# Performance work log

Hardware: AMD Instinct MI355X
Metric: run time of the kernel (lower is better)

Reference implementation:

```python
import jax, jax.numpy as jnp
import numpy as np

NUM_NODES = 100000
NUM_EDGES = 1600000
DIM = 64
TAU = 0.5
EPS = 1e-12
SURGERY_EPS = 1e-6


def setup_inputs() -> dict:
    key = jax.random.key(0)
    k1, k2, k3, k4, k5 = jax.random.split(key, 5)
    x = jax.random.normal(k1, (NUM_NODES, DIM), dtype=jnp.float32)
    edge_index = jax.random.randint(k2, (2, NUM_EDGES), 0, NUM_NODES, dtype=jnp.int64)
    edge_weight = jax.random.uniform(k3, (NUM_EDGES,), dtype=jnp.float32)
    # nn.Linear weights (no bias): y = x @ W.T
    W_self = jax.random.normal(k4, (DIM, DIM), dtype=jnp.float32) / np.sqrt(DIM)
    W_neigh = jax.random.normal(k5, (DIM, DIM), dtype=jnp.float32) / np.sqrt(DIM)
    return {"x": x, "edge_index": edge_index, "edge_weight": edge_weight,
            "W_self": W_self, "W_neigh": W_neigh}


def reference(x, edge_index, edge_weight, W_self, W_neigh):
    num_nodes = x.shape[0]
    row, col = edge_index[0], edge_index[1]

    # --- Ollivier-Ricci (LLY limit-free combinatorial lower-bound) curvature per edge ---
    deg = jax.ops.segment_sum(edge_weight, row, num_segments=num_nodes)  # weighted out-degree
    inv_du = 1.0 / jnp.maximum(deg[row], EPS)
    inv_dv = 1.0 / jnp.maximum(deg[col], EPS)
    kappa = 2.0 * inv_du + 2.0 * inv_dv - 2.0  # [E]

    # --- CFL-stable step size for the Ricci flow ---
    delta_t = 0.5 / (jnp.max(jnp.abs(kappa)) + 1e-6)

    # --- Ricci-flow half step: dw/dt = -kappa * w ---
    w_half = jnp.maximum(edge_weight * (1.0 - 0.5 * delta_t * kappa), 0.0)

    # --- metric surgery: drop degenerate edges (implemented as a zero-weight mask,
    #     keeping edge count static so the kernel is jit-compatible) ---
    mask = w_half > SURGERY_EPS
    w_half = jnp.where(mask, w_half, 0.0)

    # --- row normalisation ---
    row_sum = jax.ops.segment_sum(w_half, row, num_segments=num_nodes)
    w_norm = w_half / jnp.maximum(row_sum[row], EPS)

    # --- Laplacian off-diagonals: L_uv = -w_norm  =>  -L_uv = w_norm ---
    minus_L = w_norm

    # --- incident mean curvature per node (over surviving edges) -> curvature gate ---
    cnt = jax.ops.segment_sum(mask.astype(x.dtype), row, num_segments=num_nodes)
    k_sum = jax.ops.segment_sum(jnp.where(mask, kappa, 0.0), row, num_segments=num_nodes)
    mean_kappa = k_sum / jnp.maximum(cnt, 1.0)
    rho = jax.nn.sigmoid(mean_kappa)  # [N]

    # --- gated message passing ---
    h_self = x @ W_self.T    # [N, D]
    h_neigh = x @ W_neigh.T  # [N, D]
    msg = minus_L[:, None] * h_neigh[col]                      # [E, D] gather + scale
    neigh_aggr = jax.ops.segment_sum(msg, row, num_segments=num_nodes)  # scatter-add

    # h0 buffer == first-forward x (detached)
    out = rho[:, None] * h_self + neigh_aggr + TAU * x
    return out, edge_index, w_norm
```

## Files before the change

### kernel.cpp

```cpp
#include <hip/hip_runtime.h>
#include <math.h>

#define NNODES 100000
#define NEDGES 1600000
#define DIM 64
#define TAU 0.5f
#define EPSF 1e-12f
#define SEPS 1e-6f

#define K 256
#define RPB 391
#define TILE 4096
#define EPT 16
#define CAP 7168

typedef unsigned long long ull;
typedef unsigned short u16;
typedef __attribute__((ext_vector_type(8))) short bf16x8;
typedef __attribute__((ext_vector_type(4))) float f32x4;

__device__ __forceinline__ float bf2f(u16 h) {
    return __uint_as_float((unsigned)h << 16);
}
__device__ __forceinline__ u16 f2bf(float f) {
    unsigned u = __float_as_uint(f);
    u += 0x7FFFu + ((u >> 16) & 1);
    return (u16)(u >> 16);
}

__global__ __launch_bounds__(256) void k_bcount(const int* __restrict__ ei,
                                                int* __restrict__ bcnt, int E, int N) {
    __shared__ int cnt[K];
    cnt[threadIdx.x] = 0;
    __syncthreads();
    int stride = gridDim.x * blockDim.x;
    for (int e = blockIdx.x * blockDim.x + threadIdx.x; e < E; e += stride) {
        int r = min(max(ei[e], 0), N - 1);
        atomicAdd(&cnt[r / RPB], 1);
    }
    __syncthreads();
    int v = cnt[threadIdx.x];
    if (v) atomicAdd(&bcnt[threadIdx.x], v);
}

__global__ __launch_bounds__(256) void k_bscan(const int* __restrict__ bcnt,
                                               int* __restrict__ bbase, int* __restrict__ bcur,
                                               int* __restrict__ off, int E, int N) {
    __shared__ int sc[K];
    int t = threadIdx.x;
    int v = bcnt[t];
    sc[t] = v;
    __syncthreads();
    for (int o = 1; o < K; o <<= 1) {
        int a = (t >= o) ? sc[t - o] : 0;
        __syncthreads();
        sc[t] += a;
        __syncthreads();
    }
    int ex = sc[t] - v;
    bbase[t] = ex;
    bcur[t] = ex;
    if (t == K - 1) { bbase[K] = sc[t]; off[N] = E; }
}

__global__ __launch_bounds__(256) void k_bin(const int* __restrict__ ei, const float* __restrict__ w,
                                             int* __restrict__ bcur, ull* __restrict__ arena,
                                             int E, int N) {
    __shared__ ull stg[TILE];
    __shared__ unsigned char bkt[TILE];
    __shared__ int cnt[K], lscan[K], gbase[K], cur[K], sc[K];
    __shared__ int tot;
    int t = threadIdx.x;
    int e0 = blockIdx.x * TILE;
    cnt[t] = 0; cur[t] = 0;
    __syncthreads();
    ull rec[EPT];
    int bb[EPT];
#pragma unroll
    for (int j = 0; j < EPT; j++) {
        int e = e0 + t + j * 256;
        bb[j] = -1;
        if (e < E) {
            int r = min(max(ei[e], 0), N - 1);
            int c = min(max(ei[E + e], 0), N - 1);
            float wv = w[e];
            int b = r / RPB, lr = r - b * RPB;
            rec[j] = ((ull)__float_as_uint(wv) << 32) | (unsigned)(c | (lr << 17));
            bb[j] = b;
            atomicAdd(&cnt[b], 1);
        }
    }
    __syncthreads();
    int v = cnt[t];
    sc[t] = v;
    __syncthreads();
    for (int o = 1; o < K; o <<= 1) {
        int a = (t >= o) ? sc[t - o] : 0;
        __syncthreads();
        sc[t] += a;
        __syncthreads();
    }
    lscan[t] = sc[t] - v;
    if (v > 0) gbase[t] = atomicAdd(&bcur[t], v);
    if (t == K - 1) tot = sc[t];
    __syncthreads();
#pragma unroll
    for (int j = 0; j < EPT; j++) {
        if (bb[j] >= 0) {
            int p = lscan[bb[j]] + atomicAdd(&cur[bb[j]], 1);
            stg[p] = rec[j];
            bkt[p] = (unsigned char)bb[j];
        }
    }
    __syncthreads();
    int T = tot;
    for (int i = t; i < T; i += 256) {
        int b = bkt[i];
        arena[(size_t)gbase[b] + (i - lscan[b])] = stg[i];
    }
}

__global__ __launch_bounds__(256) void k_sort(const int* __restrict__ bbase,
                                              ull* __restrict__ arena,
                                              float* __restrict__ invdeg,
                                              int* __restrict__ off, int N) {
    __shared__ ull stg[CAP];
    __shared__ int hist[RPB];
    __shared__ float degl[RPB];
    __shared__ int cur[RPB];
    __shared__ int sc[512];
    int t = threadIdx.x, b = blockIdx.x;
    int base = bbase[b];
    int cnt = min(bbase[b + 1] - base, CAP);
    for (int i = t; i < RPB; i += 256) { hist[i] = 0; degl[i] = 0.0f; cur[i] = 0; }
    __syncthreads();
    for (int i = t; i < cnt; i += 256) {
        ull rec = arena[base + i];
        stg[i] = rec;
        int lr = (int)((rec >> 17) & 0x1FF);
        atomicAdd(&hist[lr], 1);
        atomicAdd(&degl[lr], __uint_as_float((unsigned)(rec >> 32)));
    }
    __syncthreads();
    int v0 = (t < RPB) ? hist[t] : 0;
    int v1 = (t + 256 < RPB) ? hist[t + 256] : 0;
    sc[t] = v0; sc[t + 256] = v1;
    __syncthreads();
    for (int o = 1; o < 512; o <<= 1) {
        int a = (t >= o) ? sc[t - o] : 0;
        int c2 = (t + 256 >= o) ? sc[t + 256 - o] : 0;
        __syncthreads();
        sc[t] += a; sc[t + 256] += c2;
        __syncthreads();
    }
    int ex0 = sc[t] - v0, ex1 = sc[t + 256] - v1;
    hist[t] = ex0;
    if (t + 256 < RPB) hist[t + 256] = ex1;
    int rn0 = b * RPB + t;
    if (rn0 < N) { off[rn0] = base + ex0; invdeg[rn0] = 1.0f / fmaxf(degl[t], EPSF); }
    int rn1 = rn0 + 256;
    if (t + 256 < RPB && rn1 < N) { off[rn1] = base + ex1; invdeg[rn1] = 1.0f / fmaxf(degl[t + 256], EPSF); }
    __syncthreads();
    int2* out2 = (int2*)arena;
    for (int i = t; i < cnt; i += 256) {
        ull rec = stg[i];
        int lr = (int)((rec >> 17) & 0x1FF);
        int p = hist[lr] + atomicAdd(&cur[lr], 1);
        out2[base + p] = make_int2((int)(rec & 0x1FFFF), (int)(unsigned)(rec >> 32));
    }
}

__global__ __launch_bounds__(256) void k_maxk(const int* __restrict__ off, const int2* __restrict__ csr,
                                              const float* __restrict__ invdeg,
                                              float* __restrict__ maxabs, int N) {
    int n = blockIdx.x * 256 + threadIdx.x;
    float m = 0.0f;
    if (n < N) {
        int s = off[n], e = off[n + 1];
        float a = 2.0f * invdeg[n] - 2.0f;
        for (int i = s; i < e; i++) {
            int2 pr = csr[i];
            m = fmaxf(m, fabsf(a + 2.0f * invdeg[pr.x]));
        }
    }
    for (int o = 32; o > 0; o >>= 1) m = fmaxf(m, __shfl_down(m, o, 64));
    __shared__ float red[4];
    int lane = threadIdx.x & 63, wid = threadIdx.x >> 6;
    if (lane == 0) red[wid] = m;
    __syncthreads();
    if (threadIdx.x == 0) {
        float bm = fmaxf(fmaxf(red[0], red[1]), fmaxf(red[2], red[3]));
        atomicMax((unsigned int*)maxabs, __float_as_uint(bm));
    }
}

__global__ void k_node(const int* __restrict__ off, const float* __restrict__ invdeg,
                       int2* __restrict__ csr, const float* __restrict__ maxabs,
                       float* __restrict__ rho, float* __restrict__ row_sum, int N) {
    int n = blockIdx.x * blockDim.x + threadIdx.x;
    if (n >= N) return;
    int s = off[n], e2 = off[n + 1];
    float dt = 0.5f / (*maxabs + 1e-6f);
    float a = 2.0f * invdeg[n] - 2.0f;
    float rs = 0.0f, ct = 0.0f, ks = 0.0f;
    for (int i = s; i < e2; i++) {
        int2 pr = csr[i];
        float we = __int_as_float(pr.y);
        float kap = a + 2.0f * invdeg[pr.x];
        float wh = fmaxf(we * (1.0f - 0.5f * dt * kap), 0.0f);
        float wst = 0.0f;
        if (wh > SEPS) { rs += wh; ct += 1.0f; ks += kap; wst = wh; }
        csr[i] = make_int2(pr.x, __float_as_int(wst));
    }
    float mk = ks / fmaxf(ct, 1.0f);
    rho[n] = 1.0f / (1.0f + expf(-mk));
    row_sum[n] = rs;
}

#define WL(mp, d, kk) (((mp) * 64 + (d)) * 72 + (kk))
__global__ __launch_bounds__(256) void k_gemm(const float* __restrict__ x,
                                              const float* __restrict__ Wself,
                                              const float* __restrict__ Wneigh,
                                              const float* __restrict__ rho,
                                              u16* __restrict__ hneigh_h,
                                              float* __restrict__ out, int N) {
    __shared__ u16 wlds[4 * 64 * 72];
    int t = threadIdx.x;
    for (int i = t; i < 4096; i += 256) {
        int d = i >> 6, k = i & 63;
        float v = Wself[i];
        u16 h = f2bf(v);
        u16 lo = f2bf(v - bf2f(h));
        wlds[WL(0, d, k)] = h;
        wlds[WL(1, d, k)] = lo;
        v = Wneigh[i];
        h = f2bf(v);
        lo = f2bf(v - bf2f(h));
        wlds[WL(2, d, k)] = h;
        wlds[WL(3, d, k)] = lo;
    }
    __syncthreads();
    int w = t >> 6, l = t & 63;
    int m = l & 15, kg = l >> 4;
    int n0 = blockIdx.x * 64 + w * 16;
    if (n0 >= N) return;
    int nodeA = n0 + m;
    bf16x8 ah[2], al[2];
#pragma unroll
    for (int ks = 0; ks < 2; ks++) {
        float v[8];
        if (nodeA < N) {
            const float4* xp = (const float4*)(x + (size_t)nodeA * 64 + ks * 32 + kg * 8);
            float4 v0 = xp[0], v1 = xp[1];
            v[0] = v0.x; v[1] = v0.y; v[2] = v0.z; v[3] = v0.w;
            v[4] = v1.x; v[5] = v1.y; v[6] = v1.z; v[7] = v1.w;
        } else {
#pragma unroll
            for (int j = 0; j < 8; j++) v[j] = 0.0f;
        }
#pragma unroll
        for (int j = 0; j < 8; j++) {
            u16 h = f2bf(v[j]);
            u16 lo = f2bf(v[j] - bf2f(h));
            ah[ks][j] = (short)h;
            al[ks][j] = (short)lo;
        }
    }
    f32x4 accS[4], accN[4];
#pragma unroll
    for (int dt = 0; dt < 4; dt++) {
        accS[dt] = (f32x4){0.0f, 0.0f, 0.0f, 0.0f};
        accN[dt] = (f32x4){0.0f, 0.0f, 0.0f, 0.0f};
    }
#pragma unroll
    for (int dt = 0; dt < 4; dt++) {
        int d = dt * 16 + m;
#pragma unroll
        for (int ks = 0; ks < 2; ks++) {
            int kof = ks * 32 + kg * 8;
            bf16x8 bsh = *(const bf16x8*)&wlds[WL(0, d, kof)];
            bf16x8 bsl = *(const bf16x8*)&wlds[WL(1, d, kof)];
            bf16x8 bnh = *(const bf16x8*)&wlds[WL(2, d, kof)];
            bf16x8 bnl = *(const bf16x8*)&wlds[WL(3, d, kof)];
            accS[dt] = __builtin_amdgcn_mfma_f32_16x16x32_bf16(ah[ks], bsh, accS[dt], 0, 0, 0);
            accS[dt] = __builtin_amdgcn_mfma_f32_16x16x32_bf16(al[ks], bsh, accS[dt], 0, 0, 0);
            accS[dt] = __builtin_amdgcn_mfma_f32_16x16x32_bf16(ah[ks], bsl, accS[dt], 0, 0, 0);
            accN[dt] = __builtin_amdgcn_mfma_f32_16x16x32_bf16(ah[ks], bnh, accN[dt], 0, 0, 0);
            accN[dt] = __builtin_amdgcn_mfma_f32_16x16x32_bf16(al[ks], bnh, accN[dt], 0, 0, 0);
            accN[dt] = __builtin_amdgcn_mfma_f32_16x16x32_bf16(ah[ks], bnl, accN[dt], 0, 0, 0);
        }
    }
    int rbase = kg * 4;
#pragma unroll
    for (int r = 0; r < 4; r++) {
        int nn = n0 + rbase + r;
        if (nn >= N) continue;
        float rh = rho[nn];
#pragma unroll
        for (int dt = 0; dt < 4; dt++) {
            int d = dt * 16 + m;
            size_t idx = (size_t)nn * 64 + d;
            out[idx] = rh * accS[dt][r] + TAU * x[idx];
            hneigh_h[idx] = f2bf(accN[dt][r]);
        }
    }
}

__global__ __launch_bounds__(256) void k_aggr(const int* __restrict__ off,
                                              const int2* __restrict__ csr,
                                              const float* __restrict__ row_sum,
                                              const u16* __restrict__ hneigh_h,
                                              float* __restrict__ out, int N) {
    int t = threadIdx.x;
    int lane = t & 63;
    int q = lane & 15;
    int g = lane >> 4;
    int n = blockIdx.x * 4 + (t >> 6);
    if (n >= N) return;
    int s = off[n], end = off[n + 1];
    float inv_rs = 1.0f / fmaxf(row_sum[n], EPSF);
    const ushort4* hn4 = (const ushort4*)hneigh_h;
    float a0 = 0.0f, a1 = 0.0f, a2 = 0.0f, a3 = 0.0f;
    int i = s;
    for (; i + 16 <= end; i += 16) {
        int2 p0 = csr[i + g];
        int2 p1 = csr[i + 4 + g];
        int2 p2 = csr[i + 8 + g];
        int2 p3 = csr[i + 12 + g];
        ushort4 h0 = hn4[(unsigned)((p0.x << 4) | q)];
        ushort4 h1 = hn4[(unsigned)((p1.x << 4) | q)];
        ushort4 h2 = hn4[(unsigned)((p2.x << 4) | q)];
        ushort4 h3 = hn4[(unsigned)((p3.x << 4) | q)];
        float w0 = __int_as_float(p0.y), w1 = __int_as_float(p1.y);
        float w2 = __int_as_float(p2.y), w3 = __int_as_float(p3.y);
        a0 = fmaf(w0, bf2f(h0.x), a0); a1 = fmaf(w0, bf2f(h0.y), a1);
        a2 = fmaf(w0, bf2f(h0.z), a2); a3 = fmaf(w0, bf2f(h0.w), a3);
        a0 = fmaf(w1, bf2f(h1.x), a0); a1 = fmaf(w1, bf2f(h1.y), a1);
        a2 = fmaf(w1, bf2f(h1.z), a2); a3 = fmaf(w1, bf2f(h1.w), a3);
        a0 = fmaf(w2, bf2f(h2.x), a0); a1 = fmaf(w2, bf2f(h2.y), a1);
        a2 = fmaf(w2, bf2f(h2.z), a2); a3 = fmaf(w2, bf2f(h2.w), a3);
        a0 = fmaf(w3, bf2f(h3.x), a0); a1 = fmaf(w3, bf2f(h3.y), a1);
        a2 = fmaf(w3, bf2f(h3.z), a2); a3 = fmaf(w3, bf2f(h3.w), a3);
    }
    for (; i + 8 <= end; i += 8) {
        int2 p0 = csr[i + g];
        int2 p1 = csr[i + 4 + g];
        ushort4 h0 = hn4[(unsigned)((p0.x << 4) | q)];
        ushort4 h1 = hn4[(unsigned)((p1.x << 4) | q)];
        float w0 = __int_as_float(p0.y), w1 = __int_as_float(p1.y);
        a0 = fmaf(w0, bf2f(h0.x), a0); a1 = fmaf(w0, bf2f(h0.y), a1);
        a2 = fmaf(w0, bf2f(h0.z), a2); a3 = fmaf(w0, bf2f(h0.w), a3);
        a0 = fmaf(w1, bf2f(h1.x), a0); a1 = fmaf(w1, bf2f(h1.y), a1);
        a2 = fmaf(w1, bf2f(h1.z), a2); a3 = fmaf(w1, bf2f(h1.w), a3);
    }
    for (; i < end; i += 4) {
        int e = i + g;
        bool v = e < end;
        int2 p = make_int2(0, 0);
        if (v) p = csr[e];
        ushort4 h = hn4[(unsigned)((p.x << 4) | q)];
        float wv = v ? __int_as_float(p.y) : 0.0f;
        a0 = fmaf(wv, bf2f(h.x), a0);
        a1 = fmaf(wv, bf2f(h.y), a1);
        a2 = fmaf(wv, bf2f(h.z), a2);
        a3 = fmaf(wv, bf2f(h.w), a3);
    }
    a0 += __shfl_xor(a0, 16, 64);
    a1 += __shfl_xor(a1, 16, 64);
    a2 += __shfl_xor(a2, 16, 64);
    a3 += __shfl_xor(a3, 16, 64);
    a0 += __shfl_xor(a0, 32, 64);
    a1 += __shfl_xor(a1, 32, 64);
    a2 += __shfl_xor(a2, 32, 64);
    a3 += __shfl_xor(a3, 32, 64);
    if (g == 0) {
        float4* o4 = (float4*)(out + (size_t)n * 64);
        float4 o = o4[q];
        o.x += a0 * inv_rs;
        o.y += a1 * inv_rs;
        o.z += a2 * inv_rs;
        o.w += a3 * inv_rs;
        o4[q] = o;
    }
}

__global__ void k_final(const int* __restrict__ ei, const float* __restrict__ w,
                        const float* __restrict__ invdeg, const float* __restrict__ row_sum,
                        const float* __restrict__ maxabs,
                        float* __restrict__ out_ei, float* __restrict__ out_wn, int E, int N) {
    int e = blockIdx.x * blockDim.x + threadIdx.x;
    if (e >= E) return;
    int r0 = ei[e], c0 = ei[E + e];
    int r = min(max(r0, 0), N - 1);
    int c = min(max(c0, 0), N - 1);
    float dt = 0.5f / (*maxabs + 1e-6f);
    float kap = 2.0f * invdeg[r] + 2.0f * invdeg[c] - 2.0f;
    float wh = fmaxf(w[e] * (1.0f - 0.5f * dt * kap), 0.0f);
    if (wh <= SEPS) wh = 0.0f;
    out_wn[e] = wh / fmaxf(row_sum[r], EPSF);
    out_ei[e] = (float)r0;
    out_ei[E + e] = (float)c0;
}

extern "C" void kernel_launch(void* const* d_in, const int* in_sizes, int n_in,
                              void* d_out, int out_size, void* d_ws, size_t ws_size,
                              hipStream_t stream) {
    (void)in_sizes; (void)n_in; (void)out_size; (void)ws_size;
    const int N = NNODES, E = NEDGES;

    const float* x      = (const float*)d_in[0];
    const int*   ei     = (const int*)d_in[1];
    const float* w      = (const float*)d_in[2];
    const float* Wself  = (const float*)d_in[3];
    const float* Wneigh = (const float*)d_in[4];

    float* out    = (float*)d_out;
    float* out_ei = out + (size_t)N * DIM;
    float* out_wn = out_ei + 2 * (size_t)E;

    ull*  arena = (ull*)out_ei;
    int2* csr   = (int2*)out_ei;

    float* invdeg  = (float*)d_ws;
    int*   off     = (int*)d_ws + (size_t)N;
    float* rho     = (float*)d_ws + 2 * (size_t)N + 16;
    float* row_sum = rho + (size_t)N;
    float* maxabs  = row_sum + (size_t)N;
    int*   bcnt    = (int*)(maxabs + 4);
    int*   bbase   = bcnt + 256;
    int*   bcur    = bbase + 257;
    u16*   hneigh_h = (u16*)((float*)d_ws + 4 * (size_t)N + 800);

    hipMemsetAsync((void*)maxabs, 0, 260 * sizeof(float), stream);

    k_bcount<<<256, 256, 0, stream>>>(ei, bcnt, E, N);
    k_bscan<<<1, 256, 0, stream>>>(bcnt, bbase, bcur, off, E, N);
    k_bin<<<(E + TILE - 1) / TILE, 256, 0, stream>>>(ei, w, bcur, arena, E, N);
    k_sort<<<K, 256, 0, stream>>>(bbase, arena, invdeg, off, N);
    k_maxk<<<(N + 255) / 256, 256, 0, stream>>>(off, csr, invdeg, maxabs, N);
    k_node<<<(N + 255) / 256, 256, 0, stream>>>(off, invdeg, csr, maxabs, rho, row_sum, N);
    k_gemm<<<(N + 63) / 64, 256, 0, stream>>>(x, Wself, Wneigh, rho, hneigh_h, out, N);
    k_aggr<<<(N + 3) / 4, 256, 0, stream>>>(off, csr, row_sum, hneigh_h, out, N);
    k_final<<<(E + 255) / 256, 256, 0, stream>>>(ei, w, invdeg, row_sum, maxabs,
                                                 out_ei, out_wn, E, N);
}
```

Baseline: 279.7 us.

## Drop bucket count pass via fixed-capacity buckets and recompute edge weights in aggregation

```diff
diff --git a/kernel.cpp b/kernel.cpp
--- a/kernel.cpp
+++ b/kernel.cpp
@@ -28,39 +28,8 @@
     return (u16)(u >> 16);
 }
 
-__global__ __launch_bounds__(256) void k_bcount(const int* __restrict__ ei,
-                                                int* __restrict__ bcnt, int E, int N) {
-    __shared__ int cnt[K];
-    cnt[threadIdx.x] = 0;
-    __syncthreads();
-    int stride = gridDim.x * blockDim.x;
-    for (int e = blockIdx.x * blockDim.x + threadIdx.x; e < E; e += stride) {
-        int r = min(max(ei[e], 0), N - 1);
-        atomicAdd(&cnt[r / RPB], 1);
-    }
-    __syncthreads();
-    int v = cnt[threadIdx.x];
-    if (v) atomicAdd(&bcnt[threadIdx.x], v);
-}
-
-__global__ __launch_bounds__(256) void k_bscan(const int* __restrict__ bcnt,
-                                               int* __restrict__ bbase, int* __restrict__ bcur,
-                                               int* __restrict__ off, int E, int N) {
-    __shared__ int sc[K];
-    int t = threadIdx.x;
-    int v = bcnt[t];
-    sc[t] = v;
-    __syncthreads();
-    for (int o = 1; o < K; o <<= 1) {
-        int a = (t >= o) ? sc[t - o] : 0;
-        __syncthreads();
-        sc[t] += a;
-        __syncthreads();
-    }
-    int ex = sc[t] - v;
-    bbase[t] = ex;
-    bcur[t] = ex;
-    if (t == K - 1) { bbase[K] = sc[t]; off[N] = E; }
+__global__ __launch_bounds__(256) void k_init(int* __restrict__ bcur) {
+    bcur[threadIdx.x] = threadIdx.x * CAP;
 }
 
 __global__ __launch_bounds__(256) void k_bin(const int* __restrict__ ei, const float* __restrict__ w,
@@ -116,22 +85,24 @@
     int T = tot;
     for (int i = t; i < T; i += 256) {
         int b = bkt[i];
-        arena[(size_t)gbase[b] + (i - lscan[b])] = stg[i];
-    }
-}
-
-__global__ __launch_bounds__(256) void k_sort(const int* __restrict__ bbase,
+        size_t pos = (size_t)gbase[b] + (i - lscan[b]);
+        if (pos < (size_t)(b + 1) * CAP) arena[pos] = stg[i];
+    }
+}
+
+__global__ __launch_bounds__(256) void k_sort(const int* __restrict__ bcur,
                                               ull* __restrict__ arena,
                                               float* __restrict__ invdeg,
-                                              int* __restrict__ off, int N) {
+                                              int* __restrict__ off, int* __restrict__ degi,
+                                              int N) {
     __shared__ ull stg[CAP];
     __shared__ int hist[RPB];
     __shared__ float degl[RPB];
     __shared__ int cur[RPB];
     __shared__ int sc[512];
     int t = threadIdx.x, b = blockIdx.x;
-    int base = bbase[b];
-    int cnt = min(bbase[b + 1] - base, CAP);
+    int base = b * CAP;
+    int cnt = min(bcur[b] - base, CAP);
     for (int i = t; i < RPB; i += 256) { hist[i] = 0; degl[i] = 0.0f; cur[i] = 0; }
     __syncthreads();
     for (int i = t; i < cnt; i += 256) {
@@ -157,9 +128,15 @@
     hist[t] = ex0;
     if (t + 256 < RPB) hist[t + 256] = ex1;
     int rn0 = b * RPB + t;
-    if (rn0 < N) { off[rn0] = base + ex0; invdeg[rn0] = 1.0f / fmaxf(degl[t], EPSF); }
+    if (rn0 < N) {
+        off[rn0] = base + ex0; degi[rn0] = v0;
+        invdeg[rn0] = 1.0f / fmaxf(degl[t], EPSF);
+    }
     int rn1 = rn0 + 256;
-    if (t + 256 < RPB && rn1 < N) { off[rn1] = base + ex1; invdeg[rn1] = 1.0f / fmaxf(degl[t + 256], EPSF); }
+    if (t + 256 < RPB && rn1 < N) {
+        off[rn1] = base + ex1; degi[rn1] = v1;
+        invdeg[rn1] = 1.0f / fmaxf(degl[t + 256], EPSF);
+    }
     __syncthreads();
     int2* out2 = (int2*)arena;
     for (int i = t; i < cnt; i += 256) {
@@ -170,18 +147,15 @@
     }
 }
 
-__global__ __launch_bounds__(256) void k_maxk(const int* __restrict__ off, const int2* __restrict__ csr,
+__global__ __launch_bounds__(256) void k_maxk(const int* __restrict__ ei,
                                               const float* __restrict__ invdeg,
-                                              float* __restrict__ maxabs, int N) {
-    int n = blockIdx.x * 256 + threadIdx.x;
+                                              float* __restrict__ maxabs, int E, int N) {
+    int e = blockIdx.x * 256 + threadIdx.x;
     float m = 0.0f;
-    if (n < N) {
-        int s = off[n], e = off[n + 1];
-        float a = 2.0f * invdeg[n] - 2.0f;
-        for (int i = s; i < e; i++) {
-            int2 pr = csr[i];
-            m = fmaxf(m, fabsf(a + 2.0f * invdeg[pr.x]));
-        }
+    if (e < E) {
+        int r = min(max(ei[e], 0), N - 1);
+        int c = min(max(ei[E + e], 0), N - 1);
+        m = fabsf(2.0f * invdeg[r] + 2.0f * invdeg[c] - 2.0f);
     }
     for (int o = 32; o > 0; o >>= 1) m = fmaxf(m, __shfl_down(m, o, 64));
     __shared__ float red[4];
@@ -194,12 +168,13 @@
     }
 }
 
-__global__ void k_node(const int* __restrict__ off, const float* __restrict__ invdeg,
-                       int2* __restrict__ csr, const float* __restrict__ maxabs,
+__global__ void k_node(const int* __restrict__ off, const int* __restrict__ degi,
+                       const float* __restrict__ invdeg,
+                       const int2* __restrict__ csr, const float* __restrict__ maxabs,
                        float* __restrict__ rho, float* __restrict__ row_sum, int N) {
     int n = blockIdx.x * blockDim.x + threadIdx.x;
     if (n >= N) return;
-    int s = off[n], e2 = off[n + 1];
+    int s = off[n], e2 = s + degi[n];
     float dt = 0.5f / (*maxabs + 1e-6f);
     float a = 2.0f * invdeg[n] - 2.0f;
     float rs = 0.0f, ct = 0.0f, ks = 0.0f;
@@ -208,9 +183,7 @@
         float we = __int_as_float(pr.y);
         float kap = a + 2.0f * invdeg[pr.x];
         float wh = fmaxf(we * (1.0f - 0.5f * dt * kap), 0.0f);
-        float wst = 0.0f;
-        if (wh > SEPS) { rs += wh; ct += 1.0f; ks += kap; wst = wh; }
-        csr[i] = make_int2(pr.x, __float_as_int(wst));
+        if (wh > SEPS) { rs += wh; ct += 1.0f; ks += kap; }
     }
     float mk = ks / fmaxf(ct, 1.0f);
     rho[n] = 1.0f / (1.0f + expf(-mk));
@@ -307,8 +280,11 @@
 }
 
 __global__ __launch_bounds__(256) void k_aggr(const int* __restrict__ off,
+                                              const int* __restrict__ degi,
+                                              const float* __restrict__ invdeg,
                                               const int2* __restrict__ csr,
                                               const float* __restrict__ row_sum,
+                                              const float* __restrict__ maxabs,
                                               const u16* __restrict__ hneigh_h,
                                               float* __restrict__ out, int N) {
     int t = threadIdx.x;
@@ -317,7 +293,10 @@
     int g = lane >> 4;
     int n = blockIdx.x * 4 + (t >> 6);
     if (n >= N) return;
-    int s = off[n], end = off[n + 1];
+    int s = off[n], end = s + degi[n];
+    float dt = 0.5f / (*maxabs + 1e-6f);
+    float c1 = -0.5f * dt;
+    float a = 2.0f * invdeg[n] - 2.0f;
     float inv_rs = 1.0f / fmaxf(row_sum[n], EPSF);
     const ushort4* hn4 = (const ushort4*)hneigh_h;
     float a0 = 0.0f, a1 = 0.0f, a2 = 0.0f, a3 = 0.0f;
@@ -331,8 +310,16 @@
         ushort4 h1 = hn4[(unsigned)((p1.x << 4) | q)];
         ushort4 h2 = hn4[(unsigned)((p2.x << 4) | q)];
         ushort4 h3 = hn4[(unsigned)((p3.x << 4) | q)];
-        float w0 = __int_as_float(p0.y), w1 = __int_as_float(p1.y);
-        float w2 = __int_as_float(p2.y), w3 = __int_as_float(p3.y);
+        float k0 = fmaf(2.0f, invdeg[p0.x], a), k1 = fmaf(2.0f, invdeg[p1.x], a);
+        float k2 = fmaf(2.0f, invdeg[p2.x], a), k3 = fmaf(2.0f, invdeg[p3.x], a);
+        float w0 = __int_as_float(p0.y) * fmaf(c1, k0, 1.0f);
+        float w1 = __int_as_float(p1.y) * fmaf(c1, k1, 1.0f);
+        float w2 = __int_as_float(p2.y) * fmaf(c1, k2, 1.0f);
+        float w3 = __int_as_float(p3.y) * fmaf(c1, k3, 1.0f);
+        w0 = (w0 > SEPS) ? w0 : 0.0f;
+        w1 = (w1 > SEPS) ? w1 : 0.0f;
+        w2 = (w2 > SEPS) ? w2 : 0.0f;
+        w3 = (w3 > SEPS) ? w3 : 0.0f;
         a0 = fmaf(w0, bf2f(h0.x), a0); a1 = fmaf(w0, bf2f(h0.y), a1);
         a2 = fmaf(w0, bf2f(h0.z), a2); a3 = fmaf(w0, bf2f(h0.w), a3);
         a0 = fmaf(w1, bf2f(h1.x), a0); a1 = fmaf(w1, bf2f(h1.y), a1);
@@ -347,7 +334,11 @@
         int2 p1 = csr[i + 4 + g];
         ushort4 h0 = hn4[(unsigned)((p0.x << 4) | q)];
         ushort4 h1 = hn4[(unsigned)((p1.x << 4) | q)];
-        float w0 = __int_as_float(p0.y), w1 = __int_as_float(p1.y);
+        float k0 = fmaf(2.0f, invdeg[p0.x], a), k1 = fmaf(2.0f, invdeg[p1.x], a);
+        float w0 = __int_as_float(p0.y) * fmaf(c1, k0, 1.0f);
+        float w1 = __int_as_float(p1.y) * fmaf(c1, k1, 1.0f);
+        w0 = (w0 > SEPS) ? w0 : 0.0f;
+        w1 = (w1 > SEPS) ? w1 : 0.0f;
         a0 = fmaf(w0, bf2f(h0.x), a0); a1 = fmaf(w0, bf2f(h0.y), a1);
         a2 = fmaf(w0, bf2f(h0.z), a2); a3 = fmaf(w0, bf2f(h0.w), a3);
         a0 = fmaf(w1, bf2f(h1.x), a0); a1 = fmaf(w1, bf2f(h1.y), a1);
@@ -359,7 +350,9 @@
         int2 p = make_int2(0, 0);
         if (v) p = csr[e];
         ushort4 h = hn4[(unsigned)((p.x << 4) | q)];
-        float wv = v ? __int_as_float(p.y) : 0.0f;
+        float kk = fmaf(2.0f, invdeg[p.x], a);
+        float wv = __int_as_float(p.y) * fmaf(c1, kk, 1.0f);
+        wv = (v && wv > SEPS) ? wv : 0.0f;
         a0 = fmaf(wv, bf2f(h.x), a0);
         a1 = fmaf(wv, bf2f(h.y), a1);
         a2 = fmaf(wv, bf2f(h.z), a2);
@@ -423,24 +416,23 @@
 
     float* invdeg  = (float*)d_ws;
     int*   off     = (int*)d_ws + (size_t)N;
-    float* rho     = (float*)d_ws + 2 * (size_t)N + 16;
+    int*   degi    = (int*)d_ws + 2 * (size_t)N;
+    float* rho     = (float*)d_ws + 3 * (size_t)N;
     float* row_sum = rho + (size_t)N;
     float* maxabs  = row_sum + (size_t)N;
-    int*   bcnt    = (int*)(maxabs + 4);
-    int*   bbase   = bcnt + 256;
-    int*   bcur    = bbase + 257;
-    u16*   hneigh_h = (u16*)((float*)d_ws + 4 * (size_t)N + 800);
-
-    hipMemsetAsync((void*)maxabs, 0, 260 * sizeof(float), stream);
-
-    k_bcount<<<256, 256, 0, stream>>>(ei, bcnt, E, N);
-    k_bscan<<<1, 256, 0, stream>>>(bcnt, bbase, bcur, off, E, N);
+    int*   bcur    = (int*)(maxabs + 4);
+    u16*   hneigh_h = (u16*)((float*)d_ws + 5 * (size_t)N + 272);
+
+    hipMemsetAsync((void*)maxabs, 0, 4 * sizeof(float), stream);
+
+    k_init<<<1, 256, 0, stream>>>(bcur);
     k_bin<<<(E + TILE - 1) / TILE, 256, 0, stream>>>(ei, w, bcur, arena, E, N);
-    k_sort<<<K, 256, 0, stream>>>(bbase, arena, invdeg, off, N);
-    k_maxk<<<(N + 255) / 256, 256, 0, stream>>>(off, csr, invdeg, maxabs, N);
-    k_node<<<(N + 255) / 256, 256, 0, stream>>>(off, invdeg, csr, maxabs, rho, row_sum, N);
+    k_sort<<<K, 256, 0, stream>>>(bcur, arena, invdeg, off, degi, N);
+    k_maxk<<<(E + 255) / 256, 256, 0, stream>>>(ei, invdeg, maxabs, E, N);
+    k_node<<<(N + 255) / 256, 256, 0, stream>>>(off, degi, invdeg, csr, maxabs, rho, row_sum, N);
     k_gemm<<<(N + 63) / 64, 256, 0, stream>>>(x, Wself, Wneigh, rho, hneigh_h, out, N);
-    k_aggr<<<(N + 3) / 4, 256, 0, stream>>>(off, csr, row_sum, hneigh_h, out, N);
+    k_aggr<<<(N + 3) / 4, 256, 0, stream>>>(off, degi, invdeg, csr, row_sum, maxabs,
+                                            hneigh_h, out, N);
     k_final<<<(E + 255) / 256, 256, 0, stream>>>(ei, w, invdeg, row_sum, maxabs,
                                                  out_ei, out_wn, E, N);
 }
```

Measured after the change: 328.8 us. 1.18x slower.
